# Optimization experiments

Hardware: AMD Instinct MI355X
Metric: run time of the kernel (lower is better)

## Reference

```python
import jax, jax.numpy as jnp
import numpy as np

B, N, DIN, DE, NH, DK = 4, 256, 128, 64, 8, 16


def setup_inputs() -> dict:
    key = jax.random.key(0)
    ks = jax.random.split(key, 8)
    s = 0.05
    return {
        "h": jax.random.normal(ks[0], (B, N, DIN), jnp.float32),
        "e": jax.random.normal(ks[1], (B, N, N, DE), jnp.float32),
        "mask": jnp.ones((B, N), jnp.float32),
        "WQ": jax.random.normal(ks[2], (DIN, NH * DK), jnp.float32) * s,
        "WK": jax.random.normal(ks[3], (DIN, NH * DK), jnp.float32) * s,
        "WV": jax.random.normal(ks[4], (DIN, NH * DK), jnp.float32) * s,
        "WE": jax.random.normal(ks[5], (DE, NH * DK), jnp.float32) * s,
        "WE2": jax.random.normal(ks[6], (DE, NH * DK), jnp.float32) * s,
    }


def reference(h, e, mask, WQ, WK, WV, WE, WE2):
    b, n, _ = h.shape
    Q = (h @ WQ).reshape(b, n, NH, DK)
    K = (h @ WK).reshape(b, n, NH, DK) * (float(DK) ** -0.5)
    V = (h @ WV).reshape(b, n, NH, DK)
    E = (e @ WE).reshape(b, n, n, NH, DK)
    E2 = (e @ WE2).reshape(b, n, n, NH, DK)
    # edge-augmented scores: (b, i, j, h, k)
    scores = jnp.einsum('bihk,bjhk->bijh', Q, K)[..., None] + E2
    scores = jnp.exp(jnp.clip(scores, -5.0, 5.0))
    attn_mask = mask[:, :, None, None, None] * mask[:, None, :, None, None]
    scores = scores * attn_mask
    softmax_denom = jnp.clip(scores.sum(axis=2), 1e-6, None)  # (b,i,h,k)
    scores = scores * attn_mask  # attn_dropout p=0.0 -> identity
    out = jnp.einsum('bijhk,bjhk->bihk', scores, V)
    out = out + (scores * E).sum(axis=2)
    out = out / softmax_denom
    return out.reshape(b, n, NH * DK)
```

## Files before the change

### kernel.cpp

```cpp
#include <hip/hip_runtime.h>

#define BB   4
#define NN   256
#define DIN  128
#define DE   64
#define NH   8
#define DK   16
#define CC   128

typedef __attribute__((ext_vector_type(8))) short short8;
typedef __attribute__((ext_vector_type(4))) float f32x4;

__device__ __forceinline__ unsigned short f2bfu(float f) {
    union { float f; unsigned int i; } v; v.f = f;
    unsigned int x = v.i;
    x += 0x7FFFu + ((x >> 16) & 1u);
    return (unsigned short)(x >> 16);
}

__global__ __launch_bounds__(256) void qkv_kernel(
    const float* __restrict__ h, const float* __restrict__ WQ,
    const float* __restrict__ WK, const float* __restrict__ WV,
    float* __restrict__ Qw, float* __restrict__ Kw, float* __restrict__ Vw)
{
    __shared__ float hsh[DIN];
    __shared__ float psum[4 * 384];
    const int row = blockIdx.x;
    const int t   = threadIdx.x;
    if (t < DIN) hsh[t] = h[(size_t)row * DIN + t];
    __syncthreads();

    const int cp  = t & 63;
    const int qtr = t >> 6;
    float a0=0.f,a1=0.f,b0=0.f,b1=0.f,c0=0.f,c1=0.f;
    #pragma unroll 8
    for (int dd = 0; dd < 32; ++dd) {
        const int d = qtr * 32 + dd;
        const float hd = hsh[d];
        const float2 fq = ((const float2*)WQ)[d*64 + cp];
        const float2 fk = ((const float2*)WK)[d*64 + cp];
        const float2 fv = ((const float2*)WV)[d*64 + cp];
        a0 = fmaf(hd, fq.x, a0); a1 = fmaf(hd, fq.y, a1);
        b0 = fmaf(hd, fk.x, b0); b1 = fmaf(hd, fk.y, b1);
        c0 = fmaf(hd, fv.x, c0); c1 = fmaf(hd, fv.y, c1);
    }
    float* pq = psum + qtr * 384;
    pq[      2*cp] = a0; pq[      2*cp+1] = a1;
    pq[128 + 2*cp] = b0; pq[128 + 2*cp+1] = b1;
    pq[256 + 2*cp] = c0; pq[256 + 2*cp+1] = c1;
    __syncthreads();
    if (t < CC) {
        const float q = psum[t]     + psum[384+t]     + psum[768+t]     + psum[1152+t];
        const float k = psum[128+t] + psum[384+128+t] + psum[768+128+t] + psum[1152+128+t];
        const float v = psum[256+t] + psum[384+256+t] + psum[768+256+t] + psum[1152+256+t];
        Qw[row*CC+t] = q;
        Kw[row*CC+t] = k * 0.25f;
        Vw[row*CC+t] = v;
    }
}

__global__ __launch_bounds__(256, 2) void attn_kernel(
    const float* __restrict__ e, const float* __restrict__ maskp,
    const float* __restrict__ WE, const float* __restrict__ WE2,
    const float* __restrict__ Qw, const float* __restrict__ Kw,
    const float* __restrict__ Vw, float* __restrict__ out)
{
    __shared__ __align__(16) unsigned short esh[NN*DE];
    __shared__ __align__(16) unsigned short wtsh[2*CC*DE];

    const int row  = blockIdx.x;
    const int b    = row >> 8, i = row & 255;
    const int t    = threadIdx.x;
    const int wave = t >> 6, lane = t & 63;
    const int q4   = lane >> 4;
    const int l15  = lane & 15;

    {
        const float4* src = (const float4*)(e + (size_t)row * NN * DE);
        uint4* dst = (uint4*)esh;
        #pragma unroll
        for (int r = 0; r < 8; ++r) {
            const int cidx = r*256 + t;
            const int j = cidx >> 3, ch = cidx & 7;
            const float4 f0 = src[2*cidx];
            const float4 f1 = src[2*cidx + 1];
            union { uint4 u; unsigned short s[8]; } pk;
            pk.s[0]=f2bfu(f0.x); pk.s[1]=f2bfu(f0.y); pk.s[2]=f2bfu(f0.z); pk.s[3]=f2bfu(f0.w);
            pk.s[4]=f2bfu(f1.x); pk.s[5]=f2bfu(f1.y); pk.s[6]=f2bfu(f1.z); pk.s[7]=f2bfu(f1.w);
            dst[j*8 + (ch ^ (j & 7))] = pk.u;
        }
    }
    {
        #pragma unroll
        for (int m = 0; m < 2; ++m) {
            const float2* src = (const float2*)(m ? WE2 : WE);
            unsigned short* dstm = wtsh + m * CC * DE;
            #pragma unroll
            for (int r = 0; r < 16; ++r) {
                const int idx = r*256 + t;
                const int d  = idx >> 6;
                const int c2 = (idx & 63) * 2;
                const float2 v = src[idx];
                dstm[ c2   *DE + (((d>>3) ^ ( c2   &7))*8) + (d&7)] = f2bfu(v.x);
                dstm[(c2+1)*DE + (((d>>3) ^ ((c2+1)&7))*8) + (d&7)] = f2bfu(v.y);
            }
        }
    }
    __syncthreads();

    short8 bfrag[2][2][2];
    {
        const short8* wp = (const short8*)wtsh;
        #pragma unroll
        for (int m = 0; m < 2; ++m)
        #pragma unroll
        for (int ct = 0; ct < 2; ++ct) {
            const int c = (wave*2 + ct)*16 + l15;
            #pragma unroll
            for (int ks = 0; ks < 2; ++ks) {
                const int ch = ks*4 + q4;
                bfrag[m][ct][ks] = wp[m*1024 + c*8 + (ch ^ (c & 7))];
            }
        }
    }
    __syncthreads();

    float* qk_sh   = (float*)wtsh;
    float* msk_sh  = qk_sh + NN*9;
    float* qrow_sh = msk_sh + NN;
    if (t < CC) qrow_sh[t] = Qw[(size_t)row*CC + t];
    msk_sh[t] = maskp[b*NN + t];
    __syncthreads();

    {
        const float4* kr = (const float4*)(Kw + (size_t)(b*NN + t) * CC);
        #pragma unroll
        for (int hh = 0; hh < NH; ++hh) {
            float s = 0.f;
            #pragma unroll
            for (int p = 0; p < 4; ++p) {
                const float4 kv = kr[hh*4 + p];
                const int qb = hh*16 + p*4;
                s += kv.x*qrow_sh[qb] + kv.y*qrow_sh[qb+1]
                   + kv.z*qrow_sh[qb+2] + kv.w*qrow_sh[qb+3];
            }
            qk_sh[t*9 + hh] = s;
        }
    }
    __syncthreads();

    const float mi = msk_sh[i];
    const int g0 = wave * 2;
    float acc[2] = {0.f, 0.f}, dnm[2] = {0.f, 0.f};
    const short8* ep = (const short8*)esh;

    for (int s = 0; s < 16; ++s) {
        const int ja = s*16 + l15;
        const short8 a0 = ep[ja*8 + ((q4    ) ^ (ja & 7))];
        const short8 a1 = ep[ja*8 + ((q4 + 4) ^ (ja & 7))];
        #pragma unroll
        for (int ct = 0; ct < 2; ++ct) {
            const int g = g0 + ct;
            f32x4 s2 = {0.f,0.f,0.f,0.f}, eE = {0.f,0.f,0.f,0.f};
            s2 = __builtin_amdgcn_mfma_f32_16x16x32_bf16(a0, bfrag[1][ct][0], s2, 0,0,0);
            s2 = __builtin_amdgcn_mfma_f32_16x16x32_bf16(a1, bfrag[1][ct][1], s2, 0,0,0);
            eE = __builtin_amdgcn_mfma_f32_16x16x32_bf16(a0, bfrag[0][ct][0], eE, 0,0,0);
            eE = __builtin_amdgcn_mfma_f32_16x16x32_bf16(a1, bfrag[0][ct][1], eE, 0,0,0);
            const float* vrow = Vw + (size_t)(b*NN + s*16 + q4*4) * CC + g*16 + l15;
            #pragma unroll
            for (int r = 0; r < 4; ++r) {
                const int jr = s*16 + q4*4 + r;
                float sc = qk_sh[jr*9 + g] + s2[r];
                sc = fminf(5.f, fmaxf(-5.f, sc));
                const float p  = __expf(sc);
                const float mm = mi * msk_sh[jr];
                const float s1 = p * mm;
                dnm[ct] += s1;
                const float vv = vrow[r*CC];
                acc[ct] = fmaf(s1*mm, vv + eE[r], acc[ct]);
            }
        }
    }

    #pragma unroll
    for (int ct = 0; ct < 2; ++ct) {
        float a = acc[ct], d = dnm[ct];
        a += __shfl_xor(a, 16); a += __shfl_xor(a, 32);
        d += __shfl_xor(d, 16); d += __shfl_xor(d, 32);
        acc[ct] = a; dnm[ct] = d;
    }
    if (lane < 32) {
        const int ct = lane >> 4;
        out[(size_t)row*CC + wave*32 + lane] = acc[ct] / fmaxf(dnm[ct], 1e-6f);
    }
}

extern "C" void kernel_launch(void* const* d_in, const int* in_sizes, int n_in,
                              void* d_out, int out_size, void* d_ws, size_t ws_size,
                              hipStream_t stream)
{
    const float* h    = (const float*)d_in[0];
    const float* e    = (const float*)d_in[1];
    const float* mask = (const float*)d_in[2];
    const float* WQ   = (const float*)d_in[3];
    const float* WK   = (const float*)d_in[4];
    const float* WV   = (const float*)d_in[5];
    const float* WE   = (const float*)d_in[6];
    const float* WE2  = (const float*)d_in[7];

    float* Qw = (float*)d_ws;
    float* Kw = Qw + BB*NN*CC;
    float* Vw = Kw + BB*NN*CC;

    qkv_kernel<<<BB*NN, 256, 0, stream>>>(h, WQ, WK, WV, Qw, Kw, Vw);
    attn_kernel<<<BB*NN, 256, 0, stream>>>(e, mask, WE, WE2, Qw, Kw, Vw,
                                           (float*)d_out);
}
```

Measured before the change: 162.6 us.

## Precompute bf16 MFMA weight fragments once and batch QKV rows per block

Adds a small prep kernel that converts WE/WE2 to bf16 and stores them pre-arranged in MFMA B-fragment order in the workspace. Each attention block now loads its fragments straight into registers, so the per-block conversion and the 32KB shared weight staging disappear. Shared memory per block shrinks and occupancy is raised to 3 blocks per CU. The QKV kernel processes 4 rows per block so each weight load is reused four times. This adds one extra kernel launch and more register pressure from the higher occupancy target.

```diff
diff --git a/kernel.cpp b/kernel.cpp
--- a/kernel.cpp
+++ b/kernel.cpp
@@ -18,55 +18,94 @@
     return (unsigned short)(x >> 16);
 }
 
+__global__ __launch_bounds__(256) void wprep_kernel(
+    const float* __restrict__ WE, const float* __restrict__ WE2,
+    unsigned short* __restrict__ wfrag)
+{
+    const int tid  = blockIdx.x * 256 + threadIdx.x;
+    const int m    = tid >> 10;
+    const int g    = (tid >> 7) & 7;
+    const int ks   = (tid >> 6) & 1;
+    const int lane = tid & 63;
+    const int q4 = lane >> 4, l15 = lane & 15;
+    const float* W = m ? WE2 : WE;
+    union { uint4 u; unsigned short s[8]; } pk;
+    #pragma unroll
+    for (int ii = 0; ii < 8; ++ii) {
+        const int d = ks * 32 + q4 * 8 + ii;
+        pk.s[ii] = f2bfu(W[d * CC + g * 16 + l15]);
+    }
+    ((uint4*)wfrag)[tid] = pk.u;
+}
+
 __global__ __launch_bounds__(256) void qkv_kernel(
     const float* __restrict__ h, const float* __restrict__ WQ,
     const float* __restrict__ WK, const float* __restrict__ WV,
     float* __restrict__ Qw, float* __restrict__ Kw, float* __restrict__ Vw)
 {
-    __shared__ float hsh[DIN];
-    __shared__ float psum[4 * 384];
-    const int row = blockIdx.x;
-    const int t   = threadIdx.x;
-    if (t < DIN) hsh[t] = h[(size_t)row * DIN + t];
+    __shared__ float hsh[4 * DIN];
+    __shared__ float psum[4 * 1536];
+    const int t  = threadIdx.x;
+    const int r0 = blockIdx.x * 4;
+
+    hsh[t]       = h[(size_t)r0 * DIN + t];
+    hsh[256 + t] = h[(size_t)r0 * DIN + 256 + t];
     __syncthreads();
 
     const int cp  = t & 63;
     const int qtr = t >> 6;
-    float a0=0.f,a1=0.f,b0=0.f,b1=0.f,c0=0.f,c1=0.f;
-    #pragma unroll 8
+    float aq[4][2], ak[4][2], av[4][2];
+    #pragma unroll
+    for (int r = 0; r < 4; ++r) {
+        aq[r][0]=aq[r][1]=ak[r][0]=ak[r][1]=av[r][0]=av[r][1]=0.f;
+    }
+    #pragma unroll 4
     for (int dd = 0; dd < 32; ++dd) {
         const int d = qtr * 32 + dd;
-        const float hd = hsh[d];
-        const float2 fq = ((const float2*)WQ)[d*64 + cp];
-        const float2 fk = ((const float2*)WK)[d*64 + cp];
-        const float2 fv = ((const float2*)WV)[d*64 + cp];
-        a0 = fmaf(hd, fq.x, a0); a1 = fmaf(hd, fq.y, a1);
-        b0 = fmaf(hd, fk.x, b0); b1 = fmaf(hd, fk.y, b1);
-        c0 = fmaf(hd, fv.x, c0); c1 = fmaf(hd, fv.y, c1);
-    }
-    float* pq = psum + qtr * 384;
-    pq[      2*cp] = a0; pq[      2*cp+1] = a1;
-    pq[128 + 2*cp] = b0; pq[128 + 2*cp+1] = b1;
-    pq[256 + 2*cp] = c0; pq[256 + 2*cp+1] = c1;
-    __syncthreads();
-    if (t < CC) {
-        const float q = psum[t]     + psum[384+t]     + psum[768+t]     + psum[1152+t];
-        const float k = psum[128+t] + psum[384+128+t] + psum[768+128+t] + psum[1152+128+t];
-        const float v = psum[256+t] + psum[384+256+t] + psum[768+256+t] + psum[1152+256+t];
-        Qw[row*CC+t] = q;
-        Kw[row*CC+t] = k * 0.25f;
-        Vw[row*CC+t] = v;
-    }
-}
-
-__global__ __launch_bounds__(256, 2) void attn_kernel(
+        const float2 fq = ((const float2*)WQ)[d * 64 + cp];
+        const float2 fk = ((const float2*)WK)[d * 64 + cp];
+        const float2 fv = ((const float2*)WV)[d * 64 + cp];
+        #pragma unroll
+        for (int r = 0; r < 4; ++r) {
+            const float hd = hsh[r * DIN + d];
+            aq[r][0] = fmaf(hd, fq.x, aq[r][0]); aq[r][1] = fmaf(hd, fq.y, aq[r][1]);
+            ak[r][0] = fmaf(hd, fk.x, ak[r][0]); ak[r][1] = fmaf(hd, fk.y, ak[r][1]);
+            av[r][0] = fmaf(hd, fv.x, av[r][0]); av[r][1] = fmaf(hd, fv.y, av[r][1]);
+        }
+    }
+    float* pq = psum + qtr * 1536;
+    #pragma unroll
+    for (int r = 0; r < 4; ++r) {
+        pq[r*384       + 2*cp] = aq[r][0]; pq[r*384       + 2*cp+1] = aq[r][1];
+        pq[r*384 + 128 + 2*cp] = ak[r][0]; pq[r*384 + 128 + 2*cp+1] = ak[r][1];
+        pq[r*384 + 256 + 2*cp] = av[r][0]; pq[r*384 + 256 + 2*cp+1] = av[r][1];
+    }
+    __syncthreads();
+    #pragma unroll
+    for (int k = 0; k < 6; ++k) {
+        const int o = k * 256 + t;
+        float v = psum[o] + psum[1536 + o] + psum[3072 + o] + psum[4608 + o];
+        const int r   = o / 384;
+        const int mc  = o - r * 384;
+        const int mat = mc >> 7;
+        const int c   = mc & 127;
+        const size_t idx = (size_t)(r0 + r) * CC + c;
+        if      (mat == 0) Qw[idx] = v;
+        else if (mat == 1) Kw[idx] = v * 0.25f;
+        else               Vw[idx] = v;
+    }
+}
+
+__global__ __launch_bounds__(256, 3) void attn_kernel(
     const float* __restrict__ e, const float* __restrict__ maskp,
-    const float* __restrict__ WE, const float* __restrict__ WE2,
+    const unsigned short* __restrict__ wfrag,
     const float* __restrict__ Qw, const float* __restrict__ Kw,
     const float* __restrict__ Vw, float* __restrict__ out)
 {
-    __shared__ __align__(16) unsigned short esh[NN*DE];
-    __shared__ __align__(16) unsigned short wtsh[2*CC*DE];
+    __shared__ __align__(16) unsigned short esh[NN * DE];
+    __shared__ float qk_sh[NN * 9];
+    __shared__ float msk_sh[NN];
+    __shared__ float qrow_sh[CC];
 
     const int row  = blockIdx.x;
     const int b    = row >> 8, i = row & 255;
@@ -80,87 +119,66 @@
         uint4* dst = (uint4*)esh;
         #pragma unroll
         for (int r = 0; r < 8; ++r) {
-            const int cidx = r*256 + t;
+            const int cidx = r * 256 + t;
             const int j = cidx >> 3, ch = cidx & 7;
-            const float4 f0 = src[2*cidx];
-            const float4 f1 = src[2*cidx + 1];
+            const float4 f0 = src[2 * cidx];
+            const float4 f1 = src[2 * cidx + 1];
             union { uint4 u; unsigned short s[8]; } pk;
             pk.s[0]=f2bfu(f0.x); pk.s[1]=f2bfu(f0.y); pk.s[2]=f2bfu(f0.z); pk.s[3]=f2bfu(f0.w);
             pk.s[4]=f2bfu(f1.x); pk.s[5]=f2bfu(f1.y); pk.s[6]=f2bfu(f1.z); pk.s[7]=f2bfu(f1.w);
-            dst[j*8 + (ch ^ (j & 7))] = pk.u;
-        }
-    }
-    {
-        #pragma unroll
-        for (int m = 0; m < 2; ++m) {
-            const float2* src = (const float2*)(m ? WE2 : WE);
-            unsigned short* dstm = wtsh + m * CC * DE;
-            #pragma unroll
-            for (int r = 0; r < 16; ++r) {
-                const int idx = r*256 + t;
-                const int d  = idx >> 6;
-                const int c2 = (idx & 63) * 2;
-                const float2 v = src[idx];
-                dstm[ c2   *DE + (((d>>3) ^ ( c2   &7))*8) + (d&7)] = f2bfu(v.x);
-                dstm[(c2+1)*DE + (((d>>3) ^ ((c2+1)&7))*8) + (d&7)] = f2bfu(v.y);
-            }
-        }
-    }
-    __syncthreads();
+            dst[j * 8 + (ch ^ (j & 7))] = pk.u;
+        }
+    }
+    if (t < CC) qrow_sh[t] = Qw[(size_t)row * CC + t];
+    msk_sh[t] = maskp[b * NN + t];
 
     short8 bfrag[2][2][2];
     {
-        const short8* wp = (const short8*)wtsh;
+        const uint4* wf = (const uint4*)wfrag;
         #pragma unroll
         for (int m = 0; m < 2; ++m)
         #pragma unroll
         for (int ct = 0; ct < 2; ++ct) {
-            const int c = (wave*2 + ct)*16 + l15;
+            const int g = wave * 2 + ct;
             #pragma unroll
             for (int ks = 0; ks < 2; ++ks) {
-                const int ch = ks*4 + q4;
-                bfrag[m][ct][ks] = wp[m*1024 + c*8 + (ch ^ (c & 7))];
+                union { uint4 u; short8 s8; } cv;
+                cv.u = wf[((m * 8 + g) * 2 + ks) * 64 + lane];
+                bfrag[m][ct][ks] = cv.s8;
             }
         }
     }
     __syncthreads();
 
-    float* qk_sh   = (float*)wtsh;
-    float* msk_sh  = qk_sh + NN*9;
-    float* qrow_sh = msk_sh + NN;
-    if (t < CC) qrow_sh[t] = Qw[(size_t)row*CC + t];
-    msk_sh[t] = maskp[b*NN + t];
-    __syncthreads();
-
     {
-        const float4* kr = (const float4*)(Kw + (size_t)(b*NN + t) * CC);
+        const float4* kr = (const float4*)(Kw + (size_t)(b * NN + t) * CC);
         #pragma unroll
         for (int hh = 0; hh < NH; ++hh) {
             float s = 0.f;
             #pragma unroll
             for (int p = 0; p < 4; ++p) {
-                const float4 kv = kr[hh*4 + p];
-                const int qb = hh*16 + p*4;
-                s += kv.x*qrow_sh[qb] + kv.y*qrow_sh[qb+1]
-                   + kv.z*qrow_sh[qb+2] + kv.w*qrow_sh[qb+3];
+                const float4 kv = kr[hh * 4 + p];
+                const int qb = hh * 16 + p * 4;
+                s += kv.x * qrow_sh[qb]     + kv.y * qrow_sh[qb + 1]
+                   + kv.z * qrow_sh[qb + 2] + kv.w * qrow_sh[qb + 3];
             }
-            qk_sh[t*9 + hh] = s;
+            qk_sh[t * 9 + hh] = s;
         }
     }
     __syncthreads();
 
     const float mi = msk_sh[i];
-    const int g0 = wave * 2;
     float acc[2] = {0.f, 0.f}, dnm[2] = {0.f, 0.f};
     const short8* ep = (const short8*)esh;
 
+    #pragma unroll 2
     for (int s = 0; s < 16; ++s) {
-        const int ja = s*16 + l15;
-        const short8 a0 = ep[ja*8 + ((q4    ) ^ (ja & 7))];
-        const short8 a1 = ep[ja*8 + ((q4 + 4) ^ (ja & 7))];
+        const int ja = s * 16 + l15;
+        const short8 a0 = ep[ja * 8 + ((q4    ) ^ (ja & 7))];
+        const short8 a1 = ep[ja * 8 + ((q4 + 4) ^ (ja & 7))];
         #pragma unroll
         for (int ct = 0; ct < 2; ++ct) {
-            const int g = g0 + ct;
+            const int g = wave * 2 + ct;
             f32x4 s2 = {0.f,0.f,0.f,0.f}, eE = {0.f,0.f,0.f,0.f};
             s2 = __builtin_amdgcn_mfma_f32_16x16x32_bf16(a0, bfrag[1][ct][0], s2, 0,0,0);
             s2 = __builtin_amdgcn_mfma_f32_16x16x32_bf16(a1, bfrag[1][ct][1], s2, 0,0,0);
@@ -169,15 +187,15 @@
             const float* vrow = Vw + (size_t)(b*NN + s*16 + q4*4) * CC + g*16 + l15;
             #pragma unroll
             for (int r = 0; r < 4; ++r) {
-                const int jr = s*16 + q4*4 + r;
-                float sc = qk_sh[jr*9 + g] + s2[r];
+                const int jr = s * 16 + q4 * 4 + r;
+                float sc = qk_sh[jr * 9 + g] + s2[r];
                 sc = fminf(5.f, fmaxf(-5.f, sc));
                 const float p  = __expf(sc);
                 const float mm = mi * msk_sh[jr];
                 const float s1 = p * mm;
                 dnm[ct] += s1;
-                const float vv = vrow[r*CC];
-                acc[ct] = fmaf(s1*mm, vv + eE[r], acc[ct]);
+                const float vv = vrow[r * CC];
+                acc[ct] = fmaf(s1 * mm, vv + eE[r], acc[ct]);
             }
         }
     }
@@ -191,7 +209,7 @@
     }
     if (lane < 32) {
         const int ct = lane >> 4;
-        out[(size_t)row*CC + wave*32 + lane] = acc[ct] / fmaxf(dnm[ct], 1e-6f);
+        out[(size_t)row * CC + wave * 32 + lane] = acc[ct] / fmaxf(dnm[ct], 1e-6f);
     }
 }
 
@@ -208,11 +226,13 @@
     const float* WE   = (const float*)d_in[6];
     const float* WE2  = (const float*)d_in[7];
 
-    float* Qw = (float*)d_ws;
-    float* Kw = Qw + BB*NN*CC;
-    float* Vw = Kw + BB*NN*CC;
-
-    qkv_kernel<<<BB*NN, 256, 0, stream>>>(h, WQ, WK, WV, Qw, Kw, Vw);
-    attn_kernel<<<BB*NN, 256, 0, stream>>>(e, mask, WE, WE2, Qw, Kw, Vw,
+    unsigned short* wfrag = (unsigned short*)d_ws;
+    float* Qw = (float*)((char*)d_ws + 32768);
+    float* Kw = Qw + BB * NN * CC;
+    float* Vw = Kw + BB * NN * CC;
+
+    wprep_kernel<<<8,   256, 0, stream>>>(WE, WE2, wfrag);
+    qkv_kernel <<<256,  256, 0, stream>>>(h, WQ, WK, WV, Qw, Kw, Vw);
+    attn_kernel<<<BB*NN, 256, 0, stream>>>(e, mask, wfrag, Qw, Kw, Vw,
                                            (float*)d_out);
 }
```

Measured after the change: 139.2 us. 1.17x faster.
